# Optimization experiments

Hardware: AMD Instinct MI355X
Metric: run time of the kernel (lower is better)

Reference implementation:

```python
import jax, jax.numpy as jnp
import numpy as np

N = 8192  # number of DAG nodes


def setup_inputs() -> dict:
    key = jax.random.key(0)
    k1, k2, k3 = jax.random.split(key, 3)
    thresholds = jax.random.normal(k1, (N,), dtype=jnp.float32)
    # children in [-1, N): -1 marks a leaf (no child)
    left = jax.random.randint(k2, (N,), -1, N, dtype=jnp.int32)
    right = jax.random.randint(k3, (N,), -1, N, dtype=jnp.int32)
    return {"thresholds": thresholds, "left": left, "right": right}


def reference(thresholds, left, right):
    # BFS fixed-point reachability from node 0, N sequential relaxation steps.
    n_nodes = left.shape[0]

    def step(reachable, _):
        # route children of reachable non-leaf nodes into a scatter; dump
        # inactive slots into the sentinel index n_nodes (dropped on slice)
        active_left = jnp.where(reachable & (left >= 0), left, n_nodes)
        active_right = jnp.where(reachable & (right >= 0), right, n_nodes)
        new_reachable = jnp.zeros(n_nodes + 1, dtype=jnp.bool_)
        new_reachable = new_reachable.at[active_left].set(True)
        new_reachable = new_reachable.at[active_right].set(True)
        new_reachable = new_reachable.at[0].set(True)
        return (new_reachable[:n_nodes] | reachable, None)

    init = jnp.zeros(n_nodes, dtype=jnp.bool_).at[0].set(True)
    mask, _ = jax.lax.scan(step, init, None, length=n_nodes)
    return mask
```

## Files before the change

### kernel.cpp

```cpp
#include <hip/hip_runtime.h>


#define NMAX 8192
#define BLK  1024

__global__ __launch_bounds__(BLK) void dag_reach_kernel(
    const int* __restrict__ left,
    const int* __restrict__ right,
    int* __restrict__ out,
    int n)
{
    __shared__ int sL[NMAX];
    __shared__ int sR[NMAX];
    __shared__ unsigned int reach[NMAX / 32];
    __shared__ int s_changed;

    const int tid = threadIdx.x;

    for (int i = tid; i < n; i += BLK) {
        sL[i] = left[i];
        sR[i] = right[i];
    }
    for (int i = tid; i < NMAX / 32; i += BLK) reach[i] = 0u;
    __syncthreads();
    if (tid == 0) reach[0] = 1u;

    unsigned int myExp = 0u;
    const int base = tid * 8;
    __syncthreads();

    while (true) {
        if (tid == 0) s_changed = 0;
        __syncthreads();

        unsigned int word = reach[tid >> 2];
        unsigned int pend = ((word >> ((tid & 3) * 8)) & 0xFFu) & ~myExp;

        if (pend && base < n) {
            s_changed = 1;
            myExp |= pend;
            while (pend) {
                int b = __ffs(pend) - 1;
                pend &= pend - 1;
                int node = base + b;
                if (node < n) {
                    int l = sL[node];
                    int r = sR[node];
                    if (l >= 0) atomicOr(&reach[l >> 5], 1u << (l & 31));
                    if (r >= 0) atomicOr(&reach[r >> 5], 1u << (r & 31));
                }
            }
        }
        __syncthreads();
        if (!s_changed) break;
    }

    for (int i = tid; i < n; i += BLK) {
        out[i] = (int)((reach[i >> 5] >> (i & 31)) & 1u);
    }
}

extern "C" void kernel_launch(void* const* d_in, const int* in_sizes, int n_in,
                              void* d_out, int out_size, void* d_ws, size_t ws_size,
                              hipStream_t stream)
{
    const int* left  = (const int*)d_in[1];
    const int* right = (const int*)d_in[2];
    int* out = (int*)d_out;
    const int n = in_sizes[1];

    dag_reach_kernel<<<1, BLK, 0, stream>>>(left, right, out, n);
}
```

Baseline: 72.12 us.

## Use 256 threads owning a reach word each with local re-expansion loop

Shrinks the block to 256 threads so each thread owns one 32-node reach word. Each thread now re-reads its own word through a volatile pointer and keeps expanding newly set bits until none are pending, which lets propagation advance several levels between block barriers. The per-pass flag is double-buffered so no extra barrier is needed to reset it. Left/right children are loaded with int4 vector reads and packed into one int2 shared array, and the output is written as int4. The code assumes n equals NMAX and is divisible by 4, and fewer threads means less parallel expansion within each pass.

```diff
diff --git a/kernel.cpp b/kernel.cpp
--- a/kernel.cpp
+++ b/kernel.cpp
@@ -2,7 +2,8 @@
 
 
 #define NMAX 8192
-#define BLK  1024
+#define NW   (NMAX / 32)
+#define BLK  256
 
 __global__ __launch_bounds__(BLK) void dag_reach_kernel(
     const int* __restrict__ left,
@@ -10,53 +11,72 @@
     int* __restrict__ out,
     int n)
 {
-    __shared__ int sL[NMAX];
-    __shared__ int sR[NMAX];
-    __shared__ unsigned int reach[NMAX / 32];
-    __shared__ int s_changed;
+    __shared__ int2         sLR[NMAX];
+    __shared__ unsigned int reach[NW];
+    __shared__ int          flag[2];
 
     const int tid = threadIdx.x;
 
-    for (int i = tid; i < n; i += BLK) {
-        sL[i] = left[i];
-        sR[i] = right[i];
+    {
+        const int4* l4 = (const int4*)left;
+        const int4* r4 = (const int4*)right;
+        const int nv = n / 4;
+        for (int i = tid; i < nv; i += BLK) {
+            int4 l = l4[i];
+            int4 r = r4[i];
+            int b = i * 4;
+            sLR[b + 0] = make_int2(l.x, r.x);
+            sLR[b + 1] = make_int2(l.y, r.y);
+            sLR[b + 2] = make_int2(l.z, r.z);
+            sLR[b + 3] = make_int2(l.w, r.w);
+        }
     }
-    for (int i = tid; i < NMAX / 32; i += BLK) reach[i] = 0u;
-    __syncthreads();
-    if (tid == 0) reach[0] = 1u;
-
-    unsigned int myExp = 0u;
-    const int base = tid * 8;
+    reach[tid] = (tid == 0) ? 1u : 0u;
+    if (tid < 2) flag[tid] = 0;
     __syncthreads();
 
-    while (true) {
-        if (tid == 0) s_changed = 0;
-        __syncthreads();
+    unsigned int expd = 0u;
+    const int base = tid * 32;
+    volatile unsigned int* vreach = (volatile unsigned int*)reach;
 
-        unsigned int word = reach[tid >> 2];
-        unsigned int pend = ((word >> ((tid & 3) * 8)) & 0xFFu) & ~myExp;
+    for (int pass = 0; ; ++pass) {
+        bool changed = false;
 
-        if (pend && base < n) {
-            s_changed = 1;
-            myExp |= pend;
-            while (pend) {
+        for (;;) {
+            unsigned int pend = vreach[tid] & ~expd;
+            if (!pend) break;
+            changed = true;
+            expd |= pend;
+            do {
                 int b = __ffs(pend) - 1;
                 pend &= pend - 1;
-                int node = base + b;
-                if (node < n) {
-                    int l = sL[node];
-                    int r = sR[node];
-                    if (l >= 0) atomicOr(&reach[l >> 5], 1u << (l & 31));
-                    if (r >= 0) atomicOr(&reach[r >> 5], 1u << (r & 31));
-                }
-            }
+                int2 lr = sLR[base + b];
+                if (lr.x >= 0) atomicOr(&reach[lr.x >> 5], 1u << (lr.x & 31));
+                if (lr.y >= 0) atomicOr(&reach[lr.y >> 5], 1u << (lr.y & 31));
+            } while (pend);
         }
+
+        if (changed)  flag[pass & 1] = 1;
+        if (tid == 0) flag[(pass + 1) & 1] = 0;
         __syncthreads();
-        if (!s_changed) break;
+        int f = flag[pass & 1];
+        __syncthreads();
+        if (!f) break;
     }
 
-    for (int i = tid; i < n; i += BLK) {
-        out[i] = (int)((reach[i >> 5] >> (i & 31)) & 1u);
+    {
+        int4* o4 = (int4*)out;
+        const int nv = n / 4;
+        for (int i = tid; i < nv; i += BLK) {
+            unsigned int w = reach[i >> 3];
+            int sh = (i & 7) * 4;
+            int4 v;
+            v.x = (int)((w >> (sh + 0)) & 1u);
+            v.y = (int)((w >> (sh + 1)) & 1u);
+            v.z = (int)((w >> (sh + 2)) & 1u);
+            v.w = (int)((w >> (sh + 3)) & 1u);
+            o4[i] = v;
+        }
     }
 }
 
```

Measured after the change: 84.09 us. 16.6% more time.
